# Optimization experiments

Hardware: AMD Instinct MI355X
Metric: run time of the kernel (lower is better)

The kernel has to match this reference:

```python
import jax, jax.numpy as jnp
import numpy as np

C, HEADS, K, P, S = 384, 12, 3, 1, 1
B, H, W = 8, 56, 56


def _unfold(v, k, p, s):
    # v: [B, C, Hs, Ws] -> [B, C, k*k, oh*ow], matching torch.nn.Unfold layout
    b, c, hs, ws = v.shape
    vp = jnp.pad(v, ((0, 0), (0, 0), (p, p), (p, p)))
    oh = (hs + 2 * p - k) // s + 1
    ow = (ws + 2 * p - k) // s + 1
    patches = jnp.stack(
        [vp[:, :, i:i + oh * s:s, j:j + ow * s:s] for i in range(k) for j in range(k)],
        axis=2,
    )  # [B, C, k*k, oh, ow]
    return patches.reshape(b, c, k * k, oh * ow)


def _fold(patches, out_h, out_w, k, p, s):
    # patches: [B, C, k*k, oh, ow] -> scatter-add to [B, C, out_h, out_w]
    b, c, _, oh, ow = patches.shape
    out = jnp.zeros((b, c, out_h + 2 * p, out_w + 2 * p), patches.dtype)
    for i in range(k):
        for j in range(k):
            out = out.at[:, :, i:i + oh * s:s, j:j + ow * s:s].add(patches[:, :, i * k + j])
    return out[:, :, p:p + out_h, p:p + out_w]


def setup_inputs() -> dict:
    key = jax.random.key(0)
    ks = jax.random.split(key, 6)
    sc = C ** -0.5
    return {
        "x": jax.random.normal(ks[0], (B, C, H, W), jnp.float32),
        "Wv": jax.random.normal(ks[1], (C, C), jnp.float32) * sc,
        "Wa": jax.random.normal(ks[2], (K ** 4 * HEADS, C), jnp.float32) * sc,
        "ba": jax.random.normal(ks[3], (K ** 4 * HEADS,), jnp.float32) * 0.01,
        "Wp": jax.random.normal(ks[4], (C, C), jnp.float32) * sc,
        "bp": jax.random.normal(ks[5], (C,), jnp.float32) * 0.01,
    }


def reference(x, Wv, Wa, ba, Wp, bp):
    b, c, h, w = x.shape
    hd = c // HEADS
    height = -(-h // S)
    width = -(-w // S)
    L = height * width
    x_hwc = x.transpose(0, 2, 3, 1)  # [B,H,W,C]
    # value projection, then the original's spatial transpose quirk: [B,C,W,H]
    v = jnp.einsum('bhwc,dc->bdwh', x_hwc, Wv)
    v = _unfold(v, K, P, S)  # [B, C, k*k, L]
    v = v.reshape(b, HEADS, hd, K * K, L).transpose(0, 1, 4, 3, 2)  # [B,n,L,k2,hd]
    # avgPool with kernel=stride=1 is identity
    a = jnp.einsum('bhwc,ec->bhwe', x_hwc, Wa) + ba
    a = a.reshape(b, L, HEADS, K * K, K * K).transpose(0, 2, 1, 3, 4)
    a = jax.nn.softmax(a * (hd ** -0.5), axis=-1)  # [B,n,L,k2,k2]
    out = jnp.einsum('bnlpq,bnlqd->bnlpd', a, v)  # [B,n,L,k2,hd]
    out = out.transpose(0, 1, 4, 3, 2).reshape(b, c, K * K, height, width)
    out = _fold(out, h, w, K, P, S)  # [B,C,H,W]
    out = jnp.einsum('bchw,dc->bhwd', out, Wp) + bp
    return out.transpose(0, 3, 1, 2)
```

## Files before the change

### kernel.cpp

```cpp
#include <hip/hip_runtime.h>
#include <hip/hip_bf16.h>
#include <math.h>

#define BATCH 8
#define CIN   384
#define HEADS 12
#define HGT   56
#define WID   56
#define HW    3136
#define NPIX  (BATCH*HW)
#define NVAL  384
#define NATT_W 1152
#define NQKV  1536
#define KSTEPS (CIN/32)
#define MB_TOT 196

typedef __bf16 bf16x8 __attribute__((ext_vector_type(8)));
typedef __bf16 bf16x4 __attribute__((ext_vector_type(4)));
typedef float f32x4 __attribute__((ext_vector_type(4)));
typedef uint32_t u32x4 __attribute__((ext_vector_type(4)));
typedef uint32_t u32x2 __attribute__((ext_vector_type(2)));
typedef __hip_bfloat16 hbf16;

__device__ __forceinline__ void gload_lds16(const void* g, void* l) {
  __builtin_amdgcn_global_load_lds(
      (const __attribute__((address_space(1))) void*)g,
      (__attribute__((address_space(3))) void*)l, 16, 0, 0);
}

#define NB_CONVX 9408
#define NB_WQKV  2304
#define NB_WP    576
__global__ __launch_bounds__(256) void prep_all(
    const float* __restrict__ x,
    const float* __restrict__ Wv, const float* __restrict__ Wa,
    const float* __restrict__ ba, const float* __restrict__ Wp,
    hbf16* __restrict__ xb, hbf16* __restrict__ wcat,
    float* __restrict__ bcat, hbf16* __restrict__ wpb)
{
  const int bid = blockIdx.x;
  const int tid = threadIdx.x;
  if (bid < NB_CONVX) {
    __shared__ float s[32][33];
    const int xt = bid % 98;
    const int yt = (bid / 98) % 12;
    const int b  = bid / (98 * 12);
    const int hw0 = xt * 32, c0 = yt * 32;
    const int tx = tid & 31, ty = tid >> 5;
    #pragma unroll
    for (int i = 0; i < 4; i++) {
      int c = c0 + ty + i * 8;
      s[ty + i * 8][tx] = x[((size_t)b * CIN + c) * HW + hw0 + tx];
    }
    __syncthreads();
    #pragma unroll
    for (int i = 0; i < 4; i++) {
      int hw = hw0 + ty + i * 8;
      xb[((size_t)b * HW + hw) * CIN + c0 + tx] =
          __float2bfloat16(s[tx][ty + i * 8]);
    }
  } else if (bid < NB_CONVX + NB_WQKV) {
    const int i = (bid - NB_CONVX) * 256 + tid;
    if (i < NQKV * CIN) {
      int n = i / CIN, k = i % CIN;
      float v = 0.f;
      if (n < NVAL) {
        v = Wv[(size_t)n * CIN + k];
      } else {
        int a = n - NVAL;
        int head = a / 96, r = a % 96, p = r / 10, q = r % 10;
        if (p < 9 && q < 9)
          v = Wa[(size_t)(head * 81 + p * 9 + q) * CIN + k];
      }
      wcat[i] = __float2bfloat16(v);
    }
    if (i < NQKV) {
      float bv = 0.f;
      if (i >= NVAL) {
        int a = i - NVAL;
        int head = a / 96, r = a % 96, p = r / 10, q = r % 10;
        if (p < 9 && q < 9) bv = ba[head * 81 + p * 9 + q];
      }
      bcat[i] = bv;
    }
  } else {
    const int i = (bid - NB_CONVX - NB_WQKV) * 256 + tid;
    if (i < CIN * CIN) wpb[i] = __float2bfloat16(Wp[i]);
  }
}

template<int MODE>
__global__ __launch_bounds__(256, 4) void gemm_fused(
    const hbf16* __restrict__ A_,
    const hbf16* __restrict__ Bt_,
    const float* __restrict__ bias,
    hbf16* __restrict__ ovp,
    hbf16* __restrict__ oat,
    float* __restrict__ oput)
{
  __shared__ __align__(16) char smem[33280];
  const __bf16* A  = (const __bf16*)A_;
  const __bf16* Bt = (const __bf16*)Bt_;

  const int tid  = threadIdx.x;
  const int wave = tid >> 6, lane = tid & 63;
  const int wr = wave >> 1, wc = wave & 1;
  const int l16 = lane & 15, kg = lane >> 4;

  const int NBN   = (MODE == 0) ? (NQKV / 128) : (NVAL / 128);
  const int FULLB = 8 * NBN * (MB_TOT / 8);
  int mb, nb;
  {
    const int wgid = blockIdx.x;
    if (wgid < FULLB) {
      const int xc = wgid & 7, r = wgid >> 3;
      nb = r % NBN;
      mb = (r / NBN) * 8 + xc;
    } else {
      const int l = wgid - FULLB;
      nb = l >> 2;
      mb = (MB_TOT & ~7) + (l & 3);
    }
  }
  const int m0 = mb * 128, n0 = nb * 128;

  float* biasLds = (float*)(smem + 32768);
  if (tid < 128) biasLds[tid] = bias[n0 + tid];

  const int srow = tid >> 2;
  const int skb  = (tid & 3) * 16;

  f32x4 acc[4][4] = {};

  auto stage = [&](int k0, int buf) {
    const char* gA = (const char*)(A  + (size_t)m0 * CIN + k0);
    const char* gB = (const char*)(Bt + (size_t)n0 * CIN + k0);
    char* lA = smem + buf * 16384;
    char* lB = smem + buf * 16384 + 8192;
    #pragma unroll
    for (int p = 0; p < 2; p++) {
      int row = p * 64 + srow;
      gload_lds16(gA + (size_t)row * (CIN * 2) + skb, lA + p * 4096 + wave * 1024);
      gload_lds16(gB + (size_t)row * (CIN * 2) + skb, lB + p * 4096 + wave * 1024);
    }
  };

  stage(0, 0);
  __syncthreads();

  for (int t = 0; t < KSTEPS; ++t) {
    const int buf = t & 1;
    if (t + 1 < KSTEPS) stage((t + 1) * 32, buf ^ 1);

    const __bf16* As = (const __bf16*)(smem + buf * 16384);
    const __bf16* Bs = (const __bf16*)(smem + buf * 16384 + 8192);
    bf16x8 af[4], bfr[4];
    #pragma unroll
    for (int mi = 0; mi < 4; mi++)
      af[mi] = *(const bf16x8*)(As + (wr * 64 + mi * 16 + l16) * 32 + kg * 8);
    #pragma unroll
    for (int ni = 0; ni < 4; ni++)
      bfr[ni] = *(const bf16x8*)(Bs + (wc * 64 + ni * 16 + l16) * 32 + kg * 8);
    #pragma unroll
    for (int mi = 0; mi < 4; mi++)
      #pragma unroll
      for (int ni = 0; ni < 4; ni++) {
        if (MODE == 0)
          acc[ni][mi] = __builtin_amdgcn_mfma_f32_16x16x32_bf16(
              bfr[ni], af[mi], acc[ni][mi], 0, 0, 0);
        else
          acc[mi][ni] = __builtin_amdgcn_mfma_f32_16x16x32_bf16(
              af[mi], bfr[ni], acc[mi][ni], 0, 0, 0);
      }
    __syncthreads();
  }

  if (MODE == 0) {
    __bf16* epi = (__bf16*)smem;
    #pragma unroll
    for (int ni = 0; ni < 4; ni++) {
      #pragma unroll
      for (int mi = 0; mi < 4; mi++) {
        const int m  = wr * 64 + mi * 16 + l16;
        const int nb2 = wc * 64 + ni * 16 + kg * 4;
        bf16x4 v4;
        #pragma unroll
        for (int r = 0; r < 4; r++)
          v4[r] = (__bf16)__float2bfloat16(acc[ni][mi][r] + biasLds[nb2 + r]);
        *(bf16x4*)(epi + m * 128 + (nb2 ^ ((m & 7) << 3))) = v4;
      }
    }
    __syncthreads();
    const bool isv = (n0 < NVAL);
    #pragma unroll
    for (int q = 0; q < 8; q++) {
      const int cid = q * 256 + tid;
      const int m = cid >> 4, nc = cid & 15;
      const int nloc = nc * 8;
      bf16x8 v = *(const bf16x8*)(epi + m * 128 + (nloc ^ ((m & 7) << 3)));
      const int mg = m0 + m;
      if (isv)
        *(bf16x8*)(ovp + (size_t)mg * NVAL + n0 + nloc) = v;
      else
        *(bf16x8*)(oat + (size_t)mg * NATT_W + (n0 - NVAL) + nloc) = v;
    }
  } else {
    float* epi = (float*)smem;
    #pragma unroll
    for (int p = 0; p < 2; p++) {
      if (p) __syncthreads();
      if (wr == p) {
        #pragma unroll
        for (int mi = 0; mi < 4; mi++) {
          #pragma unroll
          for (int ni = 0; ni < 4; ni++) {
            const int n  = wc * 64 + ni * 16 + l16;
            const int ml = mi * 16 + kg * 4;
            f32x4 v;
            #pragma unroll
            for (int r = 0; r < 4; r++) v[r] = acc[mi][ni][r] + biasLds[n];
            *(f32x4*)(epi + n * 64 + (ml ^ ((n & 7) << 2))) = v;
          }
        }
      }
      __syncthreads();
      #pragma unroll
      for (int q = 0; q < 8; q++) {
        const int cid = q * 256 + tid;
        const int n = cid >> 4, mc = cid & 15;
        const int ml = mc * 4;
        f32x4 v = *(const f32x4*)(epi + n * 64 + (ml ^ ((n & 7) << 2)));
        const int mg = m0 + p * 64 + ml;
        const int b = mg / HW, hw = mg % HW;
        *(f32x4*)(oput + ((size_t)b * NVAL + n0 + n) * HW + hw) = v;
      }
    }
  }
}

__global__ __launch_bounds__(256) void fold_fused(
    const hbf16* __restrict__ attnb,
    const hbf16* __restrict__ vprojb,
    hbf16* __restrict__ foldedb)
{
  __shared__ float Wl[16 * HEADS * 25];

  const int b    = blockIdx.x & 7;
  const int tile = blockIdx.x >> 3;
  const int tx = tile % 14, ty = tile / 14;
  const int x0 = tx * 4, y0 = ty * 4;
  const int bofs = b * HW;
  const int tid = threadIdx.x;
  const bool interior = (tx >= 1) && (tx <= 12) && (ty >= 1) && (ty <= 12);
  const float scale = 0.17677669529663687f;

  if (tid < 192) {
    const int pixL = tid / HEADS, head = tid - pixL * HEADS;
    const int y = y0 + (pixL >> 2), x = x0 + (pixL & 3);

    float W[25];
    #pragma unroll
    for (int k = 0; k < 25; k++) W[k] = 0.f;

    auto docenter = [&](int i, int j) {
      const int r = i * 3 + j;
      const uint32_t* rp = (const uint32_t*)(attnb +
          (size_t)(bofs + (y - i + 1) * WID + (x - j + 1)) * NATT_W +
          head * 96 + r * 10);
      uint32_t d[5];
      if ((r & 1) == 0) {
        u32x2 a0 = *(const u32x2*)(rp);
        u32x2 a1 = *(const u32x2*)(rp + 2);
        d[0] = a0[0]; d[1] = a0[1]; d[2] = a1[0]; d[3] = a1[1];
        d[4] = rp[4];
      } else {
        d[0] = rp[0];
        u32x2 a0 = *(const u32x2*)(rp + 1);
        u32x2 a1 = *(const u32x2*)(rp + 3);
        d[1] = a0[0]; d[2] = a0[1]; d[3] = a1[0]; d[4] = a1[1];
      }
      float v[9];
      #pragma unroll
      for (int u = 0; u < 4; u++) {
        v[2 * u]     = __uint_as_float(d[u] << 16) * scale;
        v[2 * u + 1] = __uint_as_float(d[u] & 0xffff0000u) * scale;
      }
      v[8] = __uint_as_float(d[4] << 16) * scale;
      float m = -1e30f;
      #pragma unroll
      for (int q = 0; q < 9; q++) m = fmaxf(m, v[q]);
      float s = 0.f;
      #pragma unroll
      for (int q = 0; q < 9; q++) { v[q] = __expf(v[q] - m); s += v[q]; }
      const float inv = 1.f / s;
      #pragma unroll
      for (int ip = 0; ip < 3; ip++)
        #pragma unroll
        for (int jp = 0; jp < 3; jp++)
          W[(ip - i + 2) * 5 + (jp - j + 2)] += v[ip * 3 + jp] * inv;
    };

    if (interior) {
      #pragma unroll
      for (int i = 0; i < 3; i++)
        #pragma unroll
        for (int j = 0; j < 3; j++)
          docenter(i, j);
    } else {
      #pragma unroll
      for (int i = 0; i < 3; i++)
        #pragma unroll
        for (int j = 0; j < 3; j++) {
          const int hh = y - i + 1, ww = x - j + 1;
          if (hh >= 0 && hh < HGT && ww >= 0 && ww < WID) docenter(i, j);
        }
    }
    float* o = &Wl[tid * 25];
    #pragma unroll
    for (int k = 0; k < 25; k++) o[k] = W[k];
  }
  __syncthreads();

  const int pixL = tid >> 4;
  const int ch16 = tid & 15;
  const int y = y0 + (pixL >> 2), x = x0 + (pixL & 3);
  const size_t pixofs = (size_t)(bofs + y * WID + x);
  const hbf16* vb0 = vprojb + (size_t)(bofs + (x - 2) * WID + (y - 2)) * NVAL;

  #pragma unroll
  for (int it = 0; it < 3; it++) {
    const int c0 = ch16 * 8 + it * 128;
    const int head = c0 >> 5;
    const float* Wp = &Wl[(pixL * HEADS + head) * 25];
    float acc[8];
    #pragma unroll
    for (int k = 0; k < 8; k++) acc[k] = 0.f;

    if (interior) {
      #pragma unroll
      for (int a = 0; a < 5; a++)
        #pragma unroll
        for (int e = 0; e < 5; e++) {
          const float w_ = Wp[a * 5 + e];
          const u32x4 vv = *(const u32x4*)(vb0 + (e * WID + a) * NVAL + c0);
          acc[0] += w_ * __uint_as_float(vv[0] << 16);
          acc[1] += w_ * __uint_as_float(vv[0] & 0xffff0000u);
          acc[2] += w_ * __uint_as_float(vv[1] << 16);
          acc[3] += w_ * __uint_as_float(vv[1] & 0xffff0000u);
          acc[4] += w_ * __uint_as_float(vv[2] << 16);
          acc[5] += w_ * __uint_as_float(vv[2] & 0xffff0000u);
          acc[6] += w_ * __uint_as_float(vv[3] << 16);
          acc[7] += w_ * __uint_as_float(vv[3] & 0xffff0000u);
        }
    } else {
      #pragma unroll
      for (int a = 0; a < 5; a++) {
        const int wi = y + a - 2;
        #pragma unroll
        for (int e = 0; e < 5; e++) {
          const int hi = x + e - 2;
          if (wi >= 0 && wi < WID && hi >= 0 && hi < HGT) {
            const float w_ = Wp[a * 5 + e];
            const u32x4 vv = *(const u32x4*)(
                vprojb + (size_t)(bofs + hi * WID + wi) * NVAL + c0);
            acc[0] += w_ * __uint_as_float(vv[0] << 16);
            acc[1] += w_ * __uint_as_float(vv[0] & 0xffff0000u);
            acc[2] += w_ * __uint_as_float(vv[1] << 16);
            acc[3] += w_ * __uint_as_float(vv[1] & 0xffff0000u);
            acc[4] += w_ * __uint_as_float(vv[2] << 16);
            acc[5] += w_ * __uint_as_float(vv[2] & 0xffff0000u);
            acc[6] += w_ * __uint_as_float(vv[3] << 16);
            acc[7] += w_ * __uint_as_float(vv[3] & 0xffff0000u);
          }
        }
      }
    }

    bf16x8 o;
    #pragma unroll
    for (int k = 0; k < 8; k++) o[k] = (__bf16)__float2bfloat16(acc[k]);
    *(bf16x8*)(foldedb + pixofs * NVAL + c0) = o;
  }
}

extern "C" void kernel_launch(void* const* d_in, const int* in_sizes, int n_in,
                              void* d_out, int out_size, void* d_ws, size_t ws_size,
                              hipStream_t stream)
{
  const float* x  = (const float*)d_in[0];
  const float* Wv = (const float*)d_in[1];
  const float* Wa = (const float*)d_in[2];
  const float* ba = (const float*)d_in[3];
  const float* Wp = (const float*)d_in[4];
  const float* bp = (const float*)d_in[5];
  float* out = (float*)d_out;

  char* w = (char*)d_ws;
  const size_t ATTN_B  = (size_t)NPIX * NATT_W * 2;
  const size_t VPROJ_B = (size_t)NPIX * NVAL * 2;
  const size_t XB_B    = (size_t)NPIX * CIN * 2;
  hbf16* attnb  = (hbf16*)w;
  hbf16* vprojb = (hbf16*)(w + ATTN_B);
  hbf16* xb     = (hbf16*)(w + ATTN_B + VPROJ_B);
  hbf16* wcat   = (hbf16*)(w + ATTN_B + VPROJ_B + XB_B);
  hbf16* wpb    = wcat + (size_t)NQKV * CIN;
  float* bcat   = (float*)(wpb + (size_t)CIN * CIN);
  hbf16* foldedb = xb;

  prep_all<<<dim3(NB_CONVX + NB_WQKV + NB_WP), 256, 0, stream>>>(
      x, Wv, Wa, ba, Wp, xb, wcat, bcat, wpb);
  gemm_fused<0><<<dim3(MB_TOT * (NQKV / 128)), 256, 0, stream>>>(
      xb, wcat, bcat, vprojb, attnb, nullptr);
  fold_fused<<<dim3(8 * 196), 256, 0, stream>>>(attnb, vprojb, foldedb);
  gemm_fused<1><<<dim3(MB_TOT * (NVAL / 128)), 256, 0, stream>>>(
      foldedb, wpb, bp, nullptr, nullptr, out);
}
```

Measured before the change: 121.3 us.

## Split fold kernel across channel groups and batch value loads per row

The fold kernel grid gains a second dimension of 3, so each block handles 4 heads (128 channels) instead of all 12. This shrinks the softmax weight phase to 64 threads and cuts shared memory per block, giving three times more blocks for occupancy. The interior accumulation now issues five vector loads per row before the FMAs, to expose memory-level parallelism. The cost is that the tile coordinates and bounds logic are recomputed in three blocks per tile, and only a quarter of threads work in the weight phase.

```diff
diff --git a/kernel.cpp b/kernel.cpp
--- a/kernel.cpp
+++ b/kernel.cpp
@@ -243,10 +243,11 @@
     const hbf16* __restrict__ vprojb,
     hbf16* __restrict__ foldedb)
 {
-  __shared__ float Wl[16 * HEADS * 25];
+  __shared__ float Wl[64 * 25];
 
   const int b    = blockIdx.x & 7;
   const int tile = blockIdx.x >> 3;
+  const int s    = blockIdx.y;
   const int tx = tile % 14, ty = tile / 14;
   const int x0 = tx * 4, y0 = ty * 4;
   const int bofs = b * HW;
@@ -254,8 +255,8 @@
   const bool interior = (tx >= 1) && (tx <= 12) && (ty >= 1) && (ty <= 12);
   const float scale = 0.17677669529663687f;
 
-  if (tid < 192) {
-    const int pixL = tid / HEADS, head = tid - pixL * HEADS;
+  if (tid < 64) {
+    const int pixL = tid >> 2, head = s * 4 + (tid & 3);
     const int y = y0 + (pixL >> 2), x = x0 + (pixL & 3);
 
     float W[25];
@@ -289,10 +290,10 @@
       float m = -1e30f;
       #pragma unroll
       for (int q = 0; q < 9; q++) m = fmaxf(m, v[q]);
-      float s = 0.f;
-      #pragma unroll
-      for (int q = 0; q < 9; q++) { v[q] = __expf(v[q] - m); s += v[q]; }
-      const float inv = 1.f / s;
+      float sum = 0.f;
+      #pragma unroll
+      for (int q = 0; q < 9; q++) { v[q] = __expf(v[q] - m); sum += v[q]; }
+      const float inv = 1.f / sum;
       #pragma unroll
       for (int ip = 0; ip < 3; ip++)
         #pragma unroll
@@ -325,24 +326,45 @@
   const int ch16 = tid & 15;
   const int y = y0 + (pixL >> 2), x = x0 + (pixL & 3);
   const size_t pixofs = (size_t)(bofs + y * WID + x);
+  const int c0 = s * 128 + ch16 * 8;
+  const float* Wp = &Wl[(pixL * 4 + (ch16 >> 2)) * 25];
   const hbf16* vb0 = vprojb + (size_t)(bofs + (x - 2) * WID + (y - 2)) * NVAL;
 
+  float acc[8];
   #pragma unroll
-  for (int it = 0; it < 3; it++) {
-    const int c0 = ch16 * 8 + it * 128;
-    const int head = c0 >> 5;
-    const float* Wp = &Wl[(pixL * HEADS + head) * 25];
-    float acc[8];
-    #pragma unroll
-    for (int k = 0; k < 8; k++) acc[k] = 0.f;
-
-    if (interior) {
+  for (int k = 0; k < 8; k++) acc[k] = 0.f;
+
+  if (interior) {
+    #pragma unroll
+    for (int e = 0; e < 5; e++) {
+      u32x4 t[5];
       #pragma unroll
       for (int a = 0; a < 5; a++)
-        #pragma unroll
-        for (int e = 0; e < 5; e++) {
+        t[a] = *(const u32x4*)(vb0 + (e * WID + a) * NVAL + c0);
+      #pragma unroll
+      for (int a = 0; a < 5; a++) {
+        const float w_ = Wp[a * 5 + e];
+        acc[0] += w_ * __uint_as_float(t[a][0] << 16);
+        acc[1] += w_ * __uint_as_float(t[a][0] & 0xffff0000u);
+        acc[2] += w_ * __uint_as_float(t[a][1] << 16);
+        acc[3] += w_ * __uint_as_float(t[a][1] & 0xffff0000u);
+        acc[4] += w_ * __uint_as_float(t[a][2] << 16);
+        acc[5] += w_ * __uint_as_float(t[a][2] & 0xffff0000u);
+        acc[6] += w_ * __uint_as_float(t[a][3] << 16);
+        acc[7] += w_ * __uint_as_float(t[a][3] & 0xffff0000u);
+      }
+    }
+  } else {
+    #pragma unroll
+    for (int e = 0; e < 5; e++) {
+      const int hi = x + e - 2;
+      #pragma unroll
+      for (int a = 0; a < 5; a++) {
+        const int wi = y + a - 2;
+        if (wi >= 0 && wi < WID && hi >= 0 && hi < HGT) {
           const float w_ = Wp[a * 5 + e];
-          const u32x4 vv = *(const u32x4*)(vb0 + (e * WID + a) * NVAL + c0);
+          const u32x4 vv = *(const u32x4*)(
+              vprojb + (size_t)(bofs + hi * WID + wi) * NVAL + c0);
           acc[0] += w_ * __uint_as_float(vv[0] << 16);
           acc[1] += w_ * __uint_as_float(vv[0] & 0xffff0000u);
           acc[2] += w_ * __uint_as_float(vv[1] << 16);
@@ -352,35 +374,14 @@
           acc[6] += w_ * __uint_as_float(vv[3] << 16);
           acc[7] += w_ * __uint_as_float(vv[3] & 0xffff0000u);
         }
-    } else {
-      #pragma unroll
-      for (int a = 0; a < 5; a++) {
-        const int wi = y + a - 2;
-        #pragma unroll
-        for (int e = 0; e < 5; e++) {
-          const int hi = x + e - 2;
-          if (wi >= 0 && wi < WID && hi >= 0 && hi < HGT) {
-            const float w_ = Wp[a * 5 + e];
-            const u32x4 vv = *(const u32x4*)(
-                vprojb + (size_t)(bofs + hi * WID + wi) * NVAL + c0);
-            acc[0] += w_ * __uint_as_float(vv[0] << 16);
-            acc[1] += w_ * __uint_as_float(vv[0] & 0xffff0000u);
-            acc[2] += w_ * __uint_as_float(vv[1] << 16);
-            acc[3] += w_ * __uint_as_float(vv[1] & 0xffff0000u);
-            acc[4] += w_ * __uint_as_float(vv[2] << 16);
-            acc[5] += w_ * __uint_as_float(vv[2] & 0xffff0000u);
-            acc[6] += w_ * __uint_as_float(vv[3] << 16);
-            acc[7] += w_ * __uint_as_float(vv[3] & 0xffff0000u);
-          }
-        }
-      }
-    }
-
-    bf16x8 o;
-    #pragma unroll
-    for (int k = 0; k < 8; k++) o[k] = (__bf16)__float2bfloat16(acc[k]);
-    *(bf16x8*)(foldedb + pixofs * NVAL + c0) = o;
-  }
+      }
+    }
+  }
+
+  bf16x8 o;
+  #pragma unroll
+  for (int k = 0; k < 8; k++) o[k] = (__bf16)__float2bfloat16(acc[k]);
+  *(bf16x8*)(foldedb + pixofs * NVAL + c0) = o;
 }
 
 extern "C" void kernel_launch(void* const* d_in, const int* in_sizes, int n_in,
@@ -411,7 +412,7 @@
       x, Wv, Wa, ba, Wp, xb, wcat, bcat, wpb);
   gemm_fused<0><<<dim3(MB_TOT * (NQKV / 128)), 256, 0, stream>>>(
       xb, wcat, bcat, vprojb, attnb, nullptr);
-  fold_fused<<<dim3(8 * 196), 256, 0, stream>>>(attnb, vprojb, foldedb);
+  fold_fused<<<dim3(8 * 196, 3), 256, 0, stream>>>(attnb, vprojb, foldedb);
   gemm_fused<1><<<dim3(MB_TOT * (NVAL / 128)), 256, 0, stream>>>(
       foldedb, wpb, bp, nullptr, nullptr, out);
 }
```

Result: faster. 114.7 us (-5.5%).
